# Kernel tuning notes

Hardware: AMD Instinct MI355X
Metric: run time of the kernel (lower is better)

The kernel has to match this reference:

```python
import jax, jax.numpy as jnp
import numpy as np

N, E = 50000, 600000
DIMS = [128, 256, 256, 256, 256, 64]  # in, h1..h4, out


def setup_inputs() -> dict:
    key = jax.random.key(0)
    ks = jax.random.split(key, 12)
    inp = {
        "x": jax.random.normal(ks[0], (N, DIMS[0]), dtype=jnp.float32),
        "edge_index": jax.random.randint(ks[1], (2, E), 0, N, dtype=jnp.int64 if jax.config.jax_enable_x64 else jnp.int32),
    }
    for i in range(5):
        fi, fo = DIMS[i], DIMS[i + 1]
        s = 1.0 / np.sqrt(fi)  # glorot-ish uniform, matching GCNConv default scale
        inp[f"W{i+1}"] = jax.random.uniform(ks[2 + 2 * i], (fi, fo), jnp.float32, -s, s)
        inp[f"b{i+1}"] = jnp.zeros((fo,), jnp.float32)
    return inp


def _gcn_norm(edge_index, n):
    # Add self-loops and compute symmetric normalization D^-1/2 (A+I) D^-1/2.
    loop = jnp.arange(n, dtype=edge_index.dtype)
    src = jnp.concatenate([edge_index[0], loop])  # [E+N]
    dst = jnp.concatenate([edge_index[1], loop])
    deg = jax.ops.segment_sum(jnp.ones_like(dst, dtype=jnp.float32), dst, num_segments=n)
    dinv = jnp.where(deg > 0, jax.lax.rsqrt(deg), 0.0)
    norm = dinv[src] * dinv[dst]  # [E+N]
    return src, dst, norm


def _gcn_layer(x, src, dst, norm, W, b, n):
    h = x @ W                       # [N, Fo] linear transform first (fewer msg bytes)
    msg = h[src] * norm[:, None]    # gather + edge-weight scale
    out = jax.ops.segment_sum(msg, dst, num_segments=n)  # scatter-add aggregate
    return out + b


def reference(x, edge_index, W1, b1, W2, b2, W3, b3, W4, b4, W5, b5):
    n = x.shape[0]
    src, dst, norm = _gcn_norm(edge_index, n)
    params = [(W1, b1), (W2, b2), (W3, b3), (W4, b4), (W5, b5)]
    h = x
    for i, (W, b) in enumerate(params):
        h = _gcn_layer(h, src, dst, norm, W, b, n)
        if i < 4:
            h = jax.nn.relu(h)  # dropout is identity in eval mode
    return h
```

## Files before the change

kernel.cpp:

```cpp
#include <hip/hip_runtime.h>
#include <stdint.h>


typedef _Float16 v8h __attribute__((ext_vector_type(8)));
typedef _Float16 v4h __attribute__((ext_vector_type(4)));
typedef _Float16 v2h __attribute__((ext_vector_type(2)));
typedef float v4f __attribute__((ext_vector_type(4)));

__global__ void count_edges(const int* __restrict__ dst, int E, int* __restrict__ counts) {
    int i = blockIdx.x * blockDim.x + threadIdx.x;
    if (i < E) atomicAdd(&counts[dst[i]], 1);
}

__global__ void block_sums(const int* __restrict__ counts, int n, int* __restrict__ partial) {
    __shared__ int red[256];
    int t = threadIdx.x;
    int i = blockIdx.x * 256 + t;
    red[t] = (i < n) ? counts[i] : 0;
    __syncthreads();
    #pragma unroll
    for (int off = 128; off > 0; off >>= 1) {
        if (t < off) red[t] += red[t + off];
        __syncthreads();
    }
    if (t == 0) partial[blockIdx.x] = red[0];
}

__global__ void scan_partials(int* __restrict__ partial, int nb, int* __restrict__ row_ptr, int n) {
    __shared__ int s[256];
    int t = threadIdx.x;
    int v = (t < nb) ? partial[t] : 0;
    s[t] = v;
    __syncthreads();
    #pragma unroll
    for (int off = 1; off < 256; off <<= 1) {
        int u = (t >= off) ? s[t - off] : 0;
        __syncthreads();
        s[t] += u;
        __syncthreads();
    }
    if (t < nb) partial[t] = s[t] - v;
    if (t == 0) row_ptr[n] = s[255];
}

__global__ void scan_final(const int* __restrict__ counts, int n, const int* __restrict__ partial,
                           int* __restrict__ row_ptr, float* __restrict__ dinv,
                           int* __restrict__ fill) {
    __shared__ int s[256];
    int t = threadIdx.x;
    int i = blockIdx.x * 256 + t;
    int c = (i < n) ? counts[i] : 0;
    s[t] = c;
    __syncthreads();
    #pragma unroll
    for (int off = 1; off < 256; off <<= 1) {
        int u = (t >= off) ? s[t - off] : 0;
        __syncthreads();
        s[t] += u;
        __syncthreads();
    }
    if (i < n) {
        row_ptr[i] = partial[blockIdx.x] + s[t] - c;
        dinv[i] = rsqrtf((float)(c + 1));
        fill[i] = 0;
    }
}

__global__ void build_csr(const int* __restrict__ src, const int* __restrict__ dst, int E,
                          const int* __restrict__ row_ptr, int* __restrict__ fill,
                          int2* __restrict__ esw, const float* __restrict__ dinv) {
    int i = blockIdx.x * blockDim.x + threadIdx.x;
    if (i < E) {
        int d = dst[i];
        int s = src[i];
        int pos = row_ptr[d] + atomicAdd(&fill[d], 1);
        esw[pos] = make_int2(s, __float_as_int(dinv[s]));
    }
}

struct SplitArgs {
    const float* W[5];
    _Float16* Wh[5];
    _Float16* Wl[5];
    int lgFI[5];
    int FO[5];
    int off[6];
};

__global__ void split_all(SplitArgs a) {
    int i = blockIdx.x * 256 + threadIdx.x;
    #pragma unroll
    for (int l = 0; l < 5; ++l) {
        if (i >= a.off[l] && i < a.off[l + 1]) {
            int j = i - a.off[l];
            int FI = 1 << a.lgFI[l];
            int c = j >> a.lgFI[l];
            int k = j & (FI - 1);
            float v = a.W[l][(size_t)k * a.FO[l] + c];
            _Float16 h = (_Float16)v;
            a.Wh[l][j] = h;
            a.Wl[l][j] = (_Float16)(v - (float)h);
        }
    }
}

__global__ __launch_bounds__(256) void agg_packed(
    const _Float16* __restrict__ inP, const int* __restrict__ row_ptr,
    const int2* __restrict__ esw, const float* __restrict__ dinv,
    _Float16* __restrict__ outH, _Float16* __restrict__ outL, int n) {
    int wid = (blockIdx.x * blockDim.x + threadIdx.x) >> 6;
    if (wid >= n) return;
    const int lane = threadIdx.x & 63;
    int e = __builtin_amdgcn_readfirstlane(row_ptr[wid]);
    const int end = __builtin_amdgcn_readfirstlane(row_ptr[wid + 1]);
    const float dd = dinv[wid];
    const _Float16* rb = inP + (size_t)lane * 8;
    float a0, a1, a2, a3;
    {
        v8h p = *(const v8h*)(rb + (size_t)wid * 512);
        a0 = dd * ((float)p[0] + (float)p[1]);
        a1 = dd * ((float)p[2] + (float)p[3]);
        a2 = dd * ((float)p[4] + (float)p[5]);
        a3 = dd * ((float)p[6] + (float)p[7]);
    }
#define GTH(q) (*(const v8h*)(rb + (size_t)(q).x * 512))
#define ACC(b, w)                                  \
    a0 += (w) * ((float)(b)[0] + (float)(b)[1]);   \
    a1 += (w) * ((float)(b)[2] + (float)(b)[3]);   \
    a2 += (w) * ((float)(b)[4] + (float)(b)[5]);   \
    a3 += (w) * ((float)(b)[6] + (float)(b)[7]);
    for (; e + 8 <= end; e += 8) {
        int2 q0 = esw[e + 0], q1 = esw[e + 1], q2 = esw[e + 2], q3 = esw[e + 3];
        int2 q4 = esw[e + 4], q5 = esw[e + 5], q6 = esw[e + 6], q7 = esw[e + 7];
        v8h b0 = GTH(q0), b1 = GTH(q1), b2 = GTH(q2), b3 = GTH(q3);
        v8h b4 = GTH(q4), b5 = GTH(q5), b6 = GTH(q6), b7 = GTH(q7);
        ACC(b0, __int_as_float(q0.y)) ACC(b1, __int_as_float(q1.y))
        ACC(b2, __int_as_float(q2.y)) ACC(b3, __int_as_float(q3.y))
        ACC(b4, __int_as_float(q4.y)) ACC(b5, __int_as_float(q5.y))
        ACC(b6, __int_as_float(q6.y)) ACC(b7, __int_as_float(q7.y))
    }
    if (e + 4 <= end) {
        int2 q0 = esw[e + 0], q1 = esw[e + 1], q2 = esw[e + 2], q3 = esw[e + 3];
        v8h b0 = GTH(q0), b1 = GTH(q1), b2 = GTH(q2), b3 = GTH(q3);
        ACC(b0, __int_as_float(q0.y)) ACC(b1, __int_as_float(q1.y))
        ACC(b2, __int_as_float(q2.y)) ACC(b3, __int_as_float(q3.y))
        e += 4;
    }
    if (e < end) {
        const int em = end - 1;
        int e1 = (e + 1 < end) ? e + 1 : em;
        int e2 = (e + 2 < end) ? e + 2 : em;
        int2 q0 = esw[e], q1 = esw[e1], q2 = esw[e2], q3 = esw[em];
        float w0 = __int_as_float(q0.y);
        float w1 = (e + 1 < end) ? __int_as_float(q1.y) : 0.f;
        float w2 = (e + 2 < end) ? __int_as_float(q2.y) : 0.f;
        float w3 = (e + 3 < end) ? __int_as_float(q3.y) : 0.f;
        v8h b0 = GTH(q0), b1 = GTH(q1), b2 = GTH(q2), b3 = GTH(q3);
        ACC(b0, w0) ACC(b1, w1) ACC(b2, w2) ACC(b3, w3)
    }
#undef GTH
#undef ACC
    size_t o = (size_t)wid * 256 + lane * 4;
    float s0 = dd * a0, s1 = dd * a1, s2 = dd * a2, s3 = dd * a3;
    _Float16 h0 = (_Float16)s0, h1 = (_Float16)s1, h2 = (_Float16)s2, h3 = (_Float16)s3;
    *(v4h*)&outH[o] = (v4h){h0, h1, h2, h3};
    *(v4h*)&outL[o] = (v4h){(_Float16)(s0 - (float)h0), (_Float16)(s1 - (float)h1),
                            (_Float16)(s2 - (float)h2), (_Float16)(s3 - (float)h3)};
}

__global__ __launch_bounds__(256) void agg_f32_128(
    const float* __restrict__ in, const int* __restrict__ row_ptr,
    const int2* __restrict__ esw, const float* __restrict__ dinv,
    _Float16* __restrict__ outH, _Float16* __restrict__ outL, int n) {
    int wid = (blockIdx.x * blockDim.x + threadIdx.x) >> 6;
    if (wid >= n) return;
    const int lane = threadIdx.x & 63;
    int e = __builtin_amdgcn_readfirstlane(row_ptr[wid]);
    const int end = __builtin_amdgcn_readfirstlane(row_ptr[wid + 1]);
    const float dd = dinv[wid];
    const float* rb = in + (size_t)lane * 2;
    float a0, a1;
    {
        float2 p = *(const float2*)(rb + (size_t)wid * 128);
        a0 = dd * p.x;
        a1 = dd * p.y;
    }
#define GTH(q) (*(const float2*)(rb + (size_t)(q).x * 128))
#define ACC(b, w) a0 += (w) * (b).x; a1 += (w) * (b).y;
    for (; e + 8 <= end; e += 8) {
        int2 q0 = esw[e + 0], q1 = esw[e + 1], q2 = esw[e + 2], q3 = esw[e + 3];
        int2 q4 = esw[e + 4], q5 = esw[e + 5], q6 = esw[e + 6], q7 = esw[e + 7];
        float2 b0 = GTH(q0), b1 = GTH(q1), b2 = GTH(q2), b3 = GTH(q3);
        float2 b4 = GTH(q4), b5 = GTH(q5), b6 = GTH(q6), b7 = GTH(q7);
        ACC(b0, __int_as_float(q0.y)) ACC(b1, __int_as_float(q1.y))
        ACC(b2, __int_as_float(q2.y)) ACC(b3, __int_as_float(q3.y))
        ACC(b4, __int_as_float(q4.y)) ACC(b5, __int_as_float(q5.y))
        ACC(b6, __int_as_float(q6.y)) ACC(b7, __int_as_float(q7.y))
    }
    if (e + 4 <= end) {
        int2 q0 = esw[e + 0], q1 = esw[e + 1], q2 = esw[e + 2], q3 = esw[e + 3];
        float2 b0 = GTH(q0), b1 = GTH(q1), b2 = GTH(q2), b3 = GTH(q3);
        ACC(b0, __int_as_float(q0.y)) ACC(b1, __int_as_float(q1.y))
        ACC(b2, __int_as_float(q2.y)) ACC(b3, __int_as_float(q3.y))
        e += 4;
    }
    if (e < end) {
        const int em = end - 1;
        int e1 = (e + 1 < end) ? e + 1 : em;
        int e2 = (e + 2 < end) ? e + 2 : em;
        int2 q0 = esw[e], q1 = esw[e1], q2 = esw[e2], q3 = esw[em];
        float w0 = __int_as_float(q0.y);
        float w1 = (e + 1 < end) ? __int_as_float(q1.y) : 0.f;
        float w2 = (e + 2 < end) ? __int_as_float(q2.y) : 0.f;
        float w3 = (e + 3 < end) ? __int_as_float(q3.y) : 0.f;
        float2 b0 = GTH(q0), b1 = GTH(q1), b2 = GTH(q2), b3 = GTH(q3);
        ACC(b0, w0) ACC(b1, w1) ACC(b2, w2) ACC(b3, w3)
    }
#undef GTH
#undef ACC
    size_t o = (size_t)wid * 128 + lane * 2;
    float s0 = dd * a0, s1 = dd * a1;
    _Float16 h0 = (_Float16)s0, h1 = (_Float16)s1;
    *(v2h*)&outH[o] = (v2h){h0, h1};
    *(v2h*)&outL[o] = (v2h){(_Float16)(s0 - (float)h0), (_Float16)(s1 - (float)h1)};
}

__global__ __launch_bounds__(256) void agg_f32_64(
    const float* __restrict__ in, const int* __restrict__ row_ptr,
    const int2* __restrict__ esw, const float* __restrict__ dinv,
    const float* __restrict__ bias, float* __restrict__ outF, int n) {
    int wid = (blockIdx.x * blockDim.x + threadIdx.x) >> 6;
    if (wid >= n) return;
    const int lane = threadIdx.x & 63;
    int e = __builtin_amdgcn_readfirstlane(row_ptr[wid]);
    const int end = __builtin_amdgcn_readfirstlane(row_ptr[wid + 1]);
    const float dd = dinv[wid];
    const float* rb = in + lane;
    float a0 = dd * rb[(size_t)wid * 64];
#define GTH(q) (rb[(size_t)(q).x * 64])
    for (; e + 8 <= end; e += 8) {
        int2 q0 = esw[e + 0], q1 = esw[e + 1], q2 = esw[e + 2], q3 = esw[e + 3];
        int2 q4 = esw[e + 4], q5 = esw[e + 5], q6 = esw[e + 6], q7 = esw[e + 7];
        float b0 = GTH(q0), b1 = GTH(q1), b2 = GTH(q2), b3 = GTH(q3);
        float b4 = GTH(q4), b5 = GTH(q5), b6 = GTH(q6), b7 = GTH(q7);
        a0 += __int_as_float(q0.y) * b0 + __int_as_float(q1.y) * b1;
        a0 += __int_as_float(q2.y) * b2 + __int_as_float(q3.y) * b3;
        a0 += __int_as_float(q4.y) * b4 + __int_as_float(q5.y) * b5;
        a0 += __int_as_float(q6.y) * b6 + __int_as_float(q7.y) * b7;
    }
    if (e + 4 <= end) {
        int2 q0 = esw[e + 0], q1 = esw[e + 1], q2 = esw[e + 2], q3 = esw[e + 3];
        float b0 = GTH(q0), b1 = GTH(q1), b2 = GTH(q2), b3 = GTH(q3);
        a0 += __int_as_float(q0.y) * b0 + __int_as_float(q1.y) * b1;
        a0 += __int_as_float(q2.y) * b2 + __int_as_float(q3.y) * b3;
        e += 4;
    }
    if (e < end) {
        const int em = end - 1;
        int e1 = (e + 1 < end) ? e + 1 : em;
        int e2 = (e + 2 < end) ? e + 2 : em;
        int2 q0 = esw[e], q1 = esw[e1], q2 = esw[e2], q3 = esw[em];
        float w0 = __int_as_float(q0.y);
        float w1 = (e + 1 < end) ? __int_as_float(q1.y) : 0.f;
        float w2 = (e + 2 < end) ? __int_as_float(q2.y) : 0.f;
        float w3 = (e + 3 < end) ? __int_as_float(q3.y) : 0.f;
        float b0 = GTH(q0), b1 = GTH(q1), b2 = GTH(q2), b3 = GTH(q3);
        a0 += w0 * b0 + w1 * b1 + w2 * b2 + w3 * b3;
    }
#undef GTH
    outF[(size_t)wid * 64 + lane] = dd * a0 + bias[lane];
}

__device__ __forceinline__ void gl_lds16(const _Float16* g, _Float16* l) {
    __builtin_amdgcn_global_load_lds(
        (const __attribute__((address_space(1))) uint32_t*)g,
        (__attribute__((address_space(3))) uint32_t*)l, 16, 0, 0);
}

template <int FI, int OUTMODE>
__global__ __launch_bounds__(256) void gemm_wide(
    const _Float16* __restrict__ Ah, const _Float16* __restrict__ Al,
    const _Float16* __restrict__ Wth, const _Float16* __restrict__ Wtl,
    const float* __restrict__ bias,
    uint32_t* __restrict__ Opk, _Float16* __restrict__ Oh, _Float16* __restrict__ Ol,
    int n) {
    constexpr int BK = 32;
    constexpr int NSTEP = FI / BK;
    __shared__ _Float16 lds[20480];
    const int m0 = blockIdx.x * 64;
    const int t = threadIdx.x;
    const int w = t >> 6;
    const int lane = t & 63;

    const int G = w * 64 + lane;
    const int arow = (G >> 6) * 16 + (G & 15), akc = ((G >> 4) & 3) * 8;
    const _Float16* sAh = Ah + (size_t)(m0 + arow) * FI + akc;
    const _Float16* sAl = Al + (size_t)(m0 + arow) * FI + akc;
    _Float16* dAh = &lds[w * 512];
    _Float16* dAl = &lds[2048 + w * 512];
    const int bq = lane & 15, bk = (lane >> 4) * 8;
    const _Float16* sB[4];
    _Float16* dBh[4];
    _Float16* dBl[4];
    #pragma unroll
    for (int q = 0; q < 4; ++q) {
        int sub = w * 4 + q;
        sB[q] = (const _Float16*)((size_t)(sub * 16 + bq) * FI + bk);
        dBh[q] = &lds[4096 + sub * 512];
        dBl[q] = &lds[12288 + sub * 512];
    }

    v4f acc[4][4];
    #pragma unroll
    for (int i = 0; i < 4; ++i)
        #pragma unroll
        for (int j = 0; j < 4; ++j) acc[i][j] = (v4f){0.f, 0.f, 0.f, 0.f};

    for (int s = 0; s < NSTEP; ++s) {
        const int ko = s * BK;
        gl_lds16(sAh + ko, dAh);
        gl_lds16(sAl + ko, dAl);
        #pragma unroll
        for (int q = 0; q < 4; ++q) {
            size_t off = (size_t)sB[q];
            gl_lds16(Wth + off + ko, dBh[q]);
            gl_lds16(Wtl + off + ko, dBl[q]);
        }
        __syncthreads();
        v8h ahf[4], alf[4], bhf[4], blf[4];
        #pragma unroll
        for (int i = 0; i < 4; ++i) {
            ahf[i] = *(const v8h*)&lds[i * 512 + lane * 8];
            alf[i] = *(const v8h*)&lds[2048 + i * 512 + lane * 8];
        }
        #pragma unroll
        for (int j = 0; j < 4; ++j) {
            bhf[j] = *(const v8h*)&lds[4096 + (w * 4 + j) * 512 + lane * 8];
            blf[j] = *(const v8h*)&lds[12288 + (w * 4 + j) * 512 + lane * 8];
        }
        #pragma unroll
        for (int i = 0; i < 4; ++i)
            #pragma unroll
            for (int j = 0; j < 4; ++j) {
                acc[i][j] = __builtin_amdgcn_mfma_f32_16x16x32_f16(ahf[i], bhf[j], acc[i][j], 0, 0, 0);
                acc[i][j] = __builtin_amdgcn_mfma_f32_16x16x32_f16(ahf[i], blf[j], acc[i][j], 0, 0, 0);
                acc[i][j] = __builtin_amdgcn_mfma_f32_16x16x32_f16(alf[i], bhf[j], acc[i][j], 0, 0, 0);
            }
        __syncthreads();
    }

    const int rl = (lane >> 4) * 4;
    const int cl = lane & 15;
    #pragma unroll
    for (int j = 0; j < 4; ++j) {
        const int gcol = w * 64 + j * 16 + cl;
        const float bv = bias[gcol];
        #pragma unroll
        for (int i = 0; i < 4; ++i) {
            const int grow = m0 + i * 16 + rl;
            #pragma unroll
            for (int r = 0; r < 4; ++r) {
                if (grow + r < n) {
                    float v = fmaxf(acc[i][j][r] + bv, 0.f);
                    _Float16 h = (_Float16)v;
                    _Float16 l = (_Float16)(v - (float)h);
                    if (OUTMODE == 0) {
                        uint32_t u = (uint32_t)__builtin_bit_cast(uint16_t, h) |
                                     ((uint32_t)__builtin_bit_cast(uint16_t, l) << 16);
                        Opk[(size_t)(grow + r) * 256 + gcol] = u;
                    } else {
                        Oh[(size_t)(grow + r) * 256 + gcol] = h;
                        Ol[(size_t)(grow + r) * 256 + gcol] = l;
                    }
                }
            }
        }
    }
}

__global__ __launch_bounds__(256) void gemm_narrow(
    const _Float16* __restrict__ Ah, const _Float16* __restrict__ Al,
    const _Float16* __restrict__ Wth, const _Float16* __restrict__ Wtl,
    float* __restrict__ Of, int n) {
    constexpr int FI = 256, FO = 64;
    __shared__ _Float16 lds[12288];
    const int m0 = blockIdx.x * 128;
    const int t = threadIdx.x;
    const int w = t >> 6;
    const int lane = t & 63;

    const int G0 = w * 128 + lane;
    const int G1 = G0 + 64;
    const int arow0 = (G0 >> 6) * 16 + (G0 & 15), akc0 = ((G0 >> 4) & 3) * 8;
    const int arow1 = (G1 >> 6) * 16 + (G1 & 15), akc1 = ((G1 >> 4) & 3) * 8;
    const _Float16* sAh0 = Ah + (size_t)(m0 + arow0) * FI + akc0;
    const _Float16* sAh1 = Ah + (size_t)(m0 + arow1) * FI + akc1;
    const _Float16* sAl0 = Al + (size_t)(m0 + arow0) * FI + akc0;
    const _Float16* sAl1 = Al + (size_t)(m0 + arow1) * FI + akc1;
    const int bcol = w * 16 + (lane & 15), bkc = (lane >> 4) * 8;
    const _Float16* sBh = Wth + (size_t)bcol * FI + bkc;
    const _Float16* sBl = Wtl + (size_t)bcol * FI + bkc;

    _Float16* dAh0 = &lds[w * 1024];
    _Float16* dAh1 = &lds[w * 1024 + 512];
    _Float16* dAl0 = &lds[4096 + w * 1024];
    _Float16* dAl1 = &lds[4096 + w * 1024 + 512];
    _Float16* dBh = &lds[8192 + w * 512];
    _Float16* dBl = &lds[10240 + w * 512];

    const int wm = w >> 1, wn = w & 1;
    v4f acc[4][2];
    #pragma unroll
    for (int i = 0; i < 4; ++i)
        #pragma unroll
        for (int j = 0; j < 2; ++j) acc[i][j] = (v4f){0.f, 0.f, 0.f, 0.f};

    for (int s = 0; s < 8; ++s) {
        const int ko = s * 32;
        gl_lds16(sAh0 + ko, dAh0);
        gl_lds16(sAh1 + ko, dAh1);
        gl_lds16(sAl0 + ko, dAl0);
        gl_lds16(sAl1 + ko, dAl1);
        gl_lds16(sBh + ko, dBh);
        gl_lds16(sBl + ko, dBl);
        __syncthreads();
        v8h ah[4], al[4], bh[2], bl[2];
        #pragma unroll
        for (int i = 0; i < 4; ++i) {
            ah[i] = *(const v8h*)&lds[(wm * 4 + i) * 512 + lane * 8];
            al[i] = *(const v8h*)&lds[4096 + (wm * 4 + i) * 512 + lane * 8];
        }
        #pragma unroll
        for (int j = 0; j < 2; ++j) {
            bh[j] = *(const v8h*)&lds[8192 + (wn * 2 + j) * 512 + lane * 8];
            bl[j] = *(const v8h*)&lds[10240 + (wn * 2 + j) * 512 + lane * 8];
        }
        #pragma unroll
        for (int i = 0; i < 4; ++i)
            #pragma unroll
            for (int j = 0; j < 2; ++j) {
                acc[i][j] = __builtin_amdgcn_mfma_f32_16x16x32_f16(ah[i], bh[j], acc[i][j], 0, 0, 0);
                acc[i][j] = __builtin_amdgcn_mfma_f32_16x16x32_f16(ah[i], bl[j], acc[i][j], 0, 0, 0);
                acc[i][j] = __builtin_amdgcn_mfma_f32_16x16x32_f16(al[i], bh[j], acc[i][j], 0, 0, 0);
            }
        __syncthreads();
    }

    const int rl = (lane >> 4) * 4;
    const int cl = lane & 15;
    #pragma unroll
    for (int j = 0; j < 2; ++j) {
        const int gcol = wn * 32 + j * 16 + cl;
        #pragma unroll
        for (int i = 0; i < 4; ++i) {
            const int grow = m0 + wm * 64 + i * 16 + rl;
            #pragma unroll
            for (int r = 0; r < 4; ++r)
                if (grow + r < n) Of[(size_t)(grow + r) * FO + gcol] = acc[i][j][r];
        }
    }
}

extern "C" void kernel_launch(void* const* d_in, const int* in_sizes, int n_in,
                              void* d_out, int out_size, void* d_ws, size_t ws_size,
                              hipStream_t stream) {
    const float* x = (const float*)d_in[0];
    const int* ei = (const int*)d_in[1];
    const int E = in_sizes[1] / 2;
    const int n = in_sizes[0] / 128;
    const int* esrc = ei;
    const int* edst = ei + E;
    const float* b[5] = {(const float*)d_in[3], (const float*)d_in[5], (const float*)d_in[7],
                         (const float*)d_in[9], (const float*)d_in[11]};
    float* out = (float*)d_out;
    const int NPAD = ((n + 127) / 128) * 128;

    char* ws = (char*)d_ws;
    auto carve = [&](size_t bytes) {
        char* p = ws;
        ws += (bytes + 255) & ~(size_t)255;
        return p;
    };
    int* counts = (int*)carve((size_t)n * 4);
    int* row_ptr = (int*)carve((size_t)(n + 1) * 4);
    int* fill = (int*)carve((size_t)n * 4);
    float* dinv = (float*)carve((size_t)n * 4);
    int* partial = (int*)carve(1024);
    int2* esw = (int2*)carve((size_t)E * 8);
    const int FIs[5] = {128, 256, 256, 256, 256};
    const int FOs[5] = {256, 256, 256, 256, 64};
    _Float16 *Wh[5], *Wl[5];
    for (int l = 0; l < 5; ++l) {
        Wh[l] = (_Float16*)carve((size_t)FIs[l] * FOs[l] * 2);
        Wl[l] = (_Float16*)carve((size_t)FIs[l] * FOs[l] * 2);
    }
    _Float16* Ah = (_Float16*)carve((size_t)NPAD * 256 * 2);
    _Float16* Al = (_Float16*)carve((size_t)NPAD * 256 * 2);
    uint32_t* Ppk = (uint32_t*)carve((size_t)NPAD * 256 * 4);
    _Float16* Bh2 = (_Float16*)Ppk;
    _Float16* Bl2 = (_Float16*)Ppk + (size_t)NPAD * 256;
    float* scratch = (float*)Ah;

    hipMemsetAsync(counts, 0, (size_t)n * 4, stream);
    count_edges<<<(E + 255) / 256, 256, 0, stream>>>(edst, E, counts);
    const int nsb = (n + 255) / 256;
    block_sums<<<nsb, 256, 0, stream>>>(counts, n, partial);
    scan_partials<<<1, 256, 0, stream>>>(partial, nsb, row_ptr, n);
    scan_final<<<nsb, 256, 0, stream>>>(counts, n, partial, row_ptr, dinv, fill);
    build_csr<<<(E + 255) / 256, 256, 0, stream>>>(esrc, edst, E, row_ptr, fill, esw, dinv);

    SplitArgs sa;
    int off = 0;
    for (int l = 0; l < 5; ++l) {
        sa.W[l] = (const float*)d_in[2 + 2 * l];
        sa.Wh[l] = Wh[l];
        sa.Wl[l] = Wl[l];
        sa.lgFI[l] = (FIs[l] == 128) ? 7 : 8;
        sa.FO[l] = FOs[l];
        sa.off[l] = off;
        off += FIs[l] * FOs[l];
    }
    sa.off[5] = off;
    split_all<<<(off + 255) / 256, 256, 0, stream>>>(sa);

    const int aggBlocks = (n + 3) / 4;
    const int gw = NPAD / 64;
    const int gn = NPAD / 128;

    agg_f32_128<<<aggBlocks, 256, 0, stream>>>(x, row_ptr, esw, dinv, Ah, Al, n);
    gemm_wide<128, 0><<<gw, 256, 0, stream>>>(Ah, Al, Wh[0], Wl[0], b[0], Ppk, nullptr, nullptr, n);
    for (int l = 1; l <= 2; ++l) {
        agg_packed<<<aggBlocks, 256, 0, stream>>>((const _Float16*)Ppk, row_ptr, esw, dinv, Ah, Al, n);
        gemm_wide<256, 0><<<gw, 256, 0, stream>>>(Ah, Al, Wh[l], Wl[l], b[l], Ppk, nullptr, nullptr, n);
    }
    agg_packed<<<aggBlocks, 256, 0, stream>>>((const _Float16*)Ppk, row_ptr, esw, dinv, Ah, Al, n);
    gemm_wide<256, 1><<<gw, 256, 0, stream>>>(Ah, Al, Wh[3], Wl[3], b[3], nullptr, Bh2, Bl2, n);
    gemm_narrow<<<gn, 256, 0, stream>>>(Bh2, Bl2, Wh[4], Wl[4], scratch, n);
    agg_f32_64<<<aggBlocks, 256, 0, stream>>>(scratch, row_ptr, esw, dinv, b[4], out, n);
}
```

Measured before the change: 669.5 us.

## Fuse sparse aggregation with dense GEMM per layer via LDS-staged tiles

Replaces the separate aggregation and wide GEMM kernels for layers 1-4 with one fused kernel. Each block aggregates 32 node rows straight into swizzled LDS as split fp16 hi/lo values, then runs the MFMA GEMM with bias and ReLU on those rows. This removes the global round trip of the aggregated Ah/Al buffers and halves the launch count. In exchange each block covers fewer rows, uses a large LDS allocation that can limit occupancy, and the gather phase runs serially before the GEMM with no overlap. Ping-pong buffers P0/P1 are used because a layer cannot overwrite its own input.

```diff
diff --git a/kernel.cpp b/kernel.cpp
--- a/kernel.cpp
+++ b/kernel.cpp
@@ -104,125 +104,301 @@
     }
 }
 
-__global__ __launch_bounds__(256) void agg_packed(
-    const _Float16* __restrict__ inP, const int* __restrict__ row_ptr,
+__device__ __forceinline__ void gl_lds16(const _Float16* g, _Float16* l) {
+    __builtin_amdgcn_global_load_lds(
+        (const __attribute__((address_space(1))) uint32_t*)g,
+        (__attribute__((address_space(3))) uint32_t*)l, 16, 0, 0);
+}
+
+template <int FI, int INMODE, int OUTMODE>
+__global__ __launch_bounds__(256) void layer_fused(
+    const void* __restrict__ in, const int* __restrict__ row_ptr,
     const int2* __restrict__ esw, const float* __restrict__ dinv,
-    _Float16* __restrict__ outH, _Float16* __restrict__ outL, int n) {
-    int wid = (blockIdx.x * blockDim.x + threadIdx.x) >> 6;
-    if (wid >= n) return;
-    const int lane = threadIdx.x & 63;
-    int e = __builtin_amdgcn_readfirstlane(row_ptr[wid]);
-    const int end = __builtin_amdgcn_readfirstlane(row_ptr[wid + 1]);
-    const float dd = dinv[wid];
-    const _Float16* rb = inP + (size_t)lane * 8;
-    float a0, a1, a2, a3;
-    {
-        v8h p = *(const v8h*)(rb + (size_t)wid * 512);
-        a0 = dd * ((float)p[0] + (float)p[1]);
-        a1 = dd * ((float)p[2] + (float)p[3]);
-        a2 = dd * ((float)p[4] + (float)p[5]);
-        a3 = dd * ((float)p[6] + (float)p[7]);
-    }
-#define GTH(q) (*(const v8h*)(rb + (size_t)(q).x * 512))
-#define ACC(b, w)                                  \
-    a0 += (w) * ((float)(b)[0] + (float)(b)[1]);   \
-    a1 += (w) * ((float)(b)[2] + (float)(b)[3]);   \
-    a2 += (w) * ((float)(b)[4] + (float)(b)[5]);   \
-    a3 += (w) * ((float)(b)[6] + (float)(b)[7]);
-    for (; e + 8 <= end; e += 8) {
-        int2 q0 = esw[e + 0], q1 = esw[e + 1], q2 = esw[e + 2], q3 = esw[e + 3];
-        int2 q4 = esw[e + 4], q5 = esw[e + 5], q6 = esw[e + 6], q7 = esw[e + 7];
-        v8h b0 = GTH(q0), b1 = GTH(q1), b2 = GTH(q2), b3 = GTH(q3);
-        v8h b4 = GTH(q4), b5 = GTH(q5), b6 = GTH(q6), b7 = GTH(q7);
-        ACC(b0, __int_as_float(q0.y)) ACC(b1, __int_as_float(q1.y))
-        ACC(b2, __int_as_float(q2.y)) ACC(b3, __int_as_float(q3.y))
-        ACC(b4, __int_as_float(q4.y)) ACC(b5, __int_as_float(q5.y))
-        ACC(b6, __int_as_float(q6.y)) ACC(b7, __int_as_float(q7.y))
-    }
-    if (e + 4 <= end) {
-        int2 q0 = esw[e + 0], q1 = esw[e + 1], q2 = esw[e + 2], q3 = esw[e + 3];
-        v8h b0 = GTH(q0), b1 = GTH(q1), b2 = GTH(q2), b3 = GTH(q3);
-        ACC(b0, __int_as_float(q0.y)) ACC(b1, __int_as_float(q1.y))
-        ACC(b2, __int_as_float(q2.y)) ACC(b3, __int_as_float(q3.y))
-        e += 4;
-    }
-    if (e < end) {
-        const int em = end - 1;
-        int e1 = (e + 1 < end) ? e + 1 : em;
-        int e2 = (e + 2 < end) ? e + 2 : em;
-        int2 q0 = esw[e], q1 = esw[e1], q2 = esw[e2], q3 = esw[em];
-        float w0 = __int_as_float(q0.y);
-        float w1 = (e + 1 < end) ? __int_as_float(q1.y) : 0.f;
-        float w2 = (e + 2 < end) ? __int_as_float(q2.y) : 0.f;
-        float w3 = (e + 3 < end) ? __int_as_float(q3.y) : 0.f;
-        v8h b0 = GTH(q0), b1 = GTH(q1), b2 = GTH(q2), b3 = GTH(q3);
-        ACC(b0, w0) ACC(b1, w1) ACC(b2, w2) ACC(b3, w3)
-    }
+    const _Float16* __restrict__ Wth, const _Float16* __restrict__ Wtl,
+    const float* __restrict__ bias,
+    uint32_t* __restrict__ Opk, _Float16* __restrict__ Oh, _Float16* __restrict__ Ol,
+    int n) {
+    constexpr int ALO = 32 * FI;
+    constexpr int BH = 64 * FI;
+    constexpr int BL = 64 * FI + 8192;
+    constexpr int NSTEP = FI / 32;
+    __shared__ _Float16 lds[64 * FI + 16384];
+    const int m0 = blockIdx.x * 32;
+    const int t = threadIdx.x;
+    const int w = t >> 6;
+    const int lane = t & 63;
+
+    for (int q = 0; q < 8; ++q) {
+        const int r = w * 8 + q;
+        const int grow = m0 + r;
+        if constexpr (INMODE == 1) {
+            float s0 = 0.f, s1 = 0.f, s2 = 0.f, s3 = 0.f;
+            if (grow < n) {
+                const _Float16* rb = (const _Float16*)in + (size_t)lane * 8;
+                int e = __builtin_amdgcn_readfirstlane(row_ptr[grow]);
+                const int end = __builtin_amdgcn_readfirstlane(row_ptr[grow + 1]);
+                const float dd = dinv[grow];
+                float a0, a1, a2, a3;
+                {
+                    v8h p = *(const v8h*)(rb + (size_t)grow * 512);
+                    a0 = dd * ((float)p[0] + (float)p[1]);
+                    a1 = dd * ((float)p[2] + (float)p[3]);
+                    a2 = dd * ((float)p[4] + (float)p[5]);
+                    a3 = dd * ((float)p[6] + (float)p[7]);
+                }
+#define GTH(qq) (*(const v8h*)(rb + (size_t)(qq).x * 512))
+#define ACC(b, wv)                                   \
+    a0 += (wv) * ((float)(b)[0] + (float)(b)[1]);    \
+    a1 += (wv) * ((float)(b)[2] + (float)(b)[3]);    \
+    a2 += (wv) * ((float)(b)[4] + (float)(b)[5]);    \
+    a3 += (wv) * ((float)(b)[6] + (float)(b)[7]);
+                for (; e + 8 <= end; e += 8) {
+                    int2 q0 = esw[e + 0], q1 = esw[e + 1], q2 = esw[e + 2], q3 = esw[e + 3];
+                    int2 q4 = esw[e + 4], q5 = esw[e + 5], q6 = esw[e + 6], q7 = esw[e + 7];
+                    v8h b0 = GTH(q0), b1 = GTH(q1), b2 = GTH(q2), b3 = GTH(q3);
+                    v8h b4 = GTH(q4), b5 = GTH(q5), b6 = GTH(q6), b7 = GTH(q7);
+                    ACC(b0, __int_as_float(q0.y)) ACC(b1, __int_as_float(q1.y))
+                    ACC(b2, __int_as_float(q2.y)) ACC(b3, __int_as_float(q3.y))
+                    ACC(b4, __int_as_float(q4.y)) ACC(b5, __int_as_float(q5.y))
+                    ACC(b6, __int_as_float(q6.y)) ACC(b7, __int_as_float(q7.y))
+                }
+                if (e + 4 <= end) {
+                    int2 q0 = esw[e + 0], q1 = esw[e + 1], q2 = esw[e + 2], q3 = esw[e + 3];
+                    v8h b0 = GTH(q0), b1 = GTH(q1), b2 = GTH(q2), b3 = GTH(q3);
+                    ACC(b0, __int_as_float(q0.y)) ACC(b1, __int_as_float(q1.y))
+                    ACC(b2, __int_as_float(q2.y)) ACC(b3, __int_as_float(q3.y))
+                    e += 4;
+                }
+                if (e < end) {
+                    const int em = end - 1;
+                    int e1 = (e + 1 < end) ? e + 1 : em;
+                    int e2 = (e + 2 < end) ? e + 2 : em;
+                    int2 q0 = esw[e], q1 = esw[e1], q2 = esw[e2], q3 = esw[em];
+                    float w0 = __int_as_float(q0.y);
+                    float w1 = (e + 1 < end) ? __int_as_float(q1.y) : 0.f;
+                    float w2 = (e + 2 < end) ? __int_as_float(q2.y) : 0.f;
+                    float w3 = (e + 3 < end) ? __int_as_float(q3.y) : 0.f;
+                    v8h b0 = GTH(q0), b1 = GTH(q1), b2 = GTH(q2), b3 = GTH(q3);
+                    ACC(b0, w0) ACC(b1, w1) ACC(b2, w2) ACC(b3, w3)
+                }
 #undef GTH
 #undef ACC
-    size_t o = (size_t)wid * 256 + lane * 4;
-    float s0 = dd * a0, s1 = dd * a1, s2 = dd * a2, s3 = dd * a3;
-    _Float16 h0 = (_Float16)s0, h1 = (_Float16)s1, h2 = (_Float16)s2, h3 = (_Float16)s3;
-    *(v4h*)&outH[o] = (v4h){h0, h1, h2, h3};
-    *(v4h*)&outL[o] = (v4h){(_Float16)(s0 - (float)h0), (_Float16)(s1 - (float)h1),
-                            (_Float16)(s2 - (float)h2), (_Float16)(s3 - (float)h3)};
-}
-
-__global__ __launch_bounds__(256) void agg_f32_128(
-    const float* __restrict__ in, const int* __restrict__ row_ptr,
-    const int2* __restrict__ esw, const float* __restrict__ dinv,
-    _Float16* __restrict__ outH, _Float16* __restrict__ outL, int n) {
-    int wid = (blockIdx.x * blockDim.x + threadIdx.x) >> 6;
-    if (wid >= n) return;
-    const int lane = threadIdx.x & 63;
-    int e = __builtin_amdgcn_readfirstlane(row_ptr[wid]);
-    const int end = __builtin_amdgcn_readfirstlane(row_ptr[wid + 1]);
-    const float dd = dinv[wid];
-    const float* rb = in + (size_t)lane * 2;
-    float a0, a1;
-    {
-        float2 p = *(const float2*)(rb + (size_t)wid * 128);
-        a0 = dd * p.x;
-        a1 = dd * p.y;
-    }
-#define GTH(q) (*(const float2*)(rb + (size_t)(q).x * 128))
-#define ACC(b, w) a0 += (w) * (b).x; a1 += (w) * (b).y;
-    for (; e + 8 <= end; e += 8) {
-        int2 q0 = esw[e + 0], q1 = esw[e + 1], q2 = esw[e + 2], q3 = esw[e + 3];
-        int2 q4 = esw[e + 4], q5 = esw[e + 5], q6 = esw[e + 6], q7 = esw[e + 7];
-        float2 b0 = GTH(q0), b1 = GTH(q1), b2 = GTH(q2), b3 = GTH(q3);
-        float2 b4 = GTH(q4), b5 = GTH(q5), b6 = GTH(q6), b7 = GTH(q7);
-        ACC(b0, __int_as_float(q0.y)) ACC(b1, __int_as_float(q1.y))
-        ACC(b2, __int_as_float(q2.y)) ACC(b3, __int_as_float(q3.y))
-        ACC(b4, __int_as_float(q4.y)) ACC(b5, __int_as_float(q5.y))
-        ACC(b6, __int_as_float(q6.y)) ACC(b7, __int_as_float(q7.y))
-    }
-    if (e + 4 <= end) {
-        int2 q0 = esw[e + 0], q1 = esw[e + 1], q2 = esw[e + 2], q3 = esw[e + 3];
-        float2 b0 = GTH(q0), b1 = GTH(q1), b2 = GTH(q2), b3 = GTH(q3);
-        ACC(b0, __int_as_float(q0.y)) ACC(b1, __int_as_float(q1.y))
-        ACC(b2, __int_as_float(q2.y)) ACC(b3, __int_as_float(q3.y))
-        e += 4;
-    }
-    if (e < end) {
-        const int em = end - 1;
-        int e1 = (e + 1 < end) ? e + 1 : em;
-        int e2 = (e + 2 < end) ? e + 2 : em;
-        int2 q0 = esw[e], q1 = esw[e1], q2 = esw[e2], q3 = esw[em];
-        float w0 = __int_as_float(q0.y);
-        float w1 = (e + 1 < end) ? __int_as_float(q1.y) : 0.f;
-        float w2 = (e + 2 < end) ? __int_as_float(q2.y) : 0.f;
-        float w3 = (e + 3 < end) ? __int_as_float(q3.y) : 0.f;
-        float2 b0 = GTH(q0), b1 = GTH(q1), b2 = GTH(q2), b3 = GTH(q3);
-        ACC(b0, w0) ACC(b1, w1) ACC(b2, w2) ACC(b3, w3)
-    }
+                s0 = dd * a0; s1 = dd * a1; s2 = dd * a2; s3 = dd * a3;
+            }
+            _Float16 h0 = (_Float16)s0, h1 = (_Float16)s1, h2 = (_Float16)s2, h3 = (_Float16)s3;
+            const int idx = (r * 256 + lane * 4) ^ ((r & 7) << 3);
+            *(v4h*)&lds[idx] = (v4h){h0, h1, h2, h3};
+            *(v4h*)&lds[ALO + idx] = (v4h){(_Float16)(s0 - (float)h0), (_Float16)(s1 - (float)h1),
+                                           (_Float16)(s2 - (float)h2), (_Float16)(s3 - (float)h3)};
+        } else {
+            float s0 = 0.f, s1 = 0.f;
+            if (grow < n) {
+                const float* rb = (const float*)in + (size_t)lane * 2;
+                int e = __builtin_amdgcn_readfirstlane(row_ptr[grow]);
+                const int end = __builtin_amdgcn_readfirstlane(row_ptr[grow + 1]);
+                const float dd = dinv[grow];
+                float a0, a1;
+                {
+                    float2 p = *(const float2*)(rb + (size_t)grow * 128);
+                    a0 = dd * p.x;
+                    a1 = dd * p.y;
+                }
+#define GTH(qq) (*(const float2*)(rb + (size_t)(qq).x * 128))
+#define ACC(b, wv) a0 += (wv) * (b).x; a1 += (wv) * (b).y;
+                for (; e + 8 <= end; e += 8) {
+                    int2 q0 = esw[e + 0], q1 = esw[e + 1], q2 = esw[e + 2], q3 = esw[e + 3];
+                    int2 q4 = esw[e + 4], q5 = esw[e + 5], q6 = esw[e + 6], q7 = esw[e + 7];
+                    float2 b0 = GTH(q0), b1 = GTH(q1), b2 = GTH(q2), b3 = GTH(q3);
+                    float2 b4 = GTH(q4), b5 = GTH(q5), b6 = GTH(q6), b7 = GTH(q7);
+                    ACC(b0, __int_as_float(q0.y)) ACC(b1, __int_as_float(q1.y))
+                    ACC(b2, __int_as_float(q2.y)) ACC(b3, __int_as_float(q3.y))
+                    ACC(b4, __int_as_float(q4.y)) ACC(b5, __int_as_float(q5.y))
+                    ACC(b6, __int_as_float(q6.y)) ACC(b7, __int_as_float(q7.y))
+                }
+                if (e + 4 <= end) {
+                    int2 q0 = esw[e + 0], q1 = esw[e + 1], q2 = esw[e + 2], q3 = esw[e + 3];
+                    float2 b0 = GTH(q0), b1 = GTH(q1), b2 = GTH(q2), b3 = GTH(q3);
+                    ACC(b0, __int_as_float(q0.y)) ACC(b1, __int_as_float(q1.y))
+                    ACC(b2, __int_as_float(q2.y)) ACC(b3, __int_as_float(q3.y))
+                    e += 4;
+                }
+                if (e < end) {
+                    const int em = end - 1;
+                    int e1 = (e + 1 < end) ? e + 1 : em;
+                    int e2 = (e + 2 < end) ? e + 2 : em;
+                    int2 q0 = esw[e], q1 = esw[e1], q2 = esw[e2], q3 = esw[em];
+                    float w0 = __int_as_float(q0.y);
+                    float w1 = (e + 1 < end) ? __int_as_float(q1.y) : 0.f;
+                    float w2 = (e + 2 < end) ? __int_as_float(q2.y) : 0.f;
+                    float w3 = (e + 3 < end) ? __int_as_float(q3.y) : 0.f;
+                    float2 b0 = GTH(q0), b1 = GTH(q1), b2 = GTH(q2), b3 = GTH(q3);
+                    ACC(b0, w0) ACC(b1, w1) ACC(b2, w2) ACC(b3, w3)
+                }
 #undef GTH
 #undef ACC
-    size_t o = (size_t)wid * 128 + lane * 2;
-    float s0 = dd * a0, s1 = dd * a1;
-    _Float16 h0 = (_Float16)s0, h1 = (_Float16)s1;
-    *(v2h*)&outH[o] = (v2h){h0, h1};
-    *(v2h*)&outL[o] = (v2h){(_Float16)(s0 - (float)h0), (_Float16)(s1 - (float)h1)};
+                s0 = dd * a0; s1 = dd * a1;
+            }
+            _Float16 h0 = (_Float16)s0, h1 = (_Float16)s1;
+            const int idx = (r * 128 + lane * 2) ^ ((r & 7) << 3);
+            *(v2h*)&lds[idx] = (v2h){h0, h1};
+            *(v2h*)&lds[ALO + idx] = (v2h){(_Float16)(s0 - (float)h0), (_Float16)(s1 - (float)h1)};
+        }
+    }
+    __syncthreads();
+
+    size_t boff[4];
+    #pragma unroll
+    for (int q = 0; q < 4; ++q)
+        boff[q] = (size_t)((w * 4 + q) * 16 + (lane & 15)) * FI + ((lane >> 4) * 8);
+
+    v4f acc[2][4];
+    #pragma unroll
+    for (int i = 0; i < 2; ++i)
+        #pragma unroll
+        for (int j = 0; j < 4; ++j) acc[i][j] = (v4f){0.f, 0.f, 0.f, 0.f};
+
+    for (int s = 0; s < NSTEP; ++s) {
+        const int ko = s * 32;
+        #pragma unroll
+        for (int q = 0; q < 4; ++q) {
+            gl_lds16(Wth + boff[q] + ko, &lds[BH + (w * 4 + q) * 512]);
+            gl_lds16(Wtl + boff[q] + ko, &lds[BL + (w * 4 + q) * 512]);
+        }
+        __syncthreads();
+        v8h ahf[2], alf[2], bhf[4], blf[4];
+        #pragma unroll
+        for (int i = 0; i < 2; ++i) {
+            const int ri = i * 16 + (lane & 15);
+            const int aidx = (ri * FI + ko + ((lane >> 4) << 3)) ^ ((lane & 7) << 3);
+            ahf[i] = *(const v8h*)&lds[aidx];
+            alf[i] = *(const v8h*)&lds[ALO + aidx];
+        }
+        #pragma unroll
+        for (int j = 0; j < 4; ++j) {
+            bhf[j] = *(const v8h*)&lds[BH + (w * 4 + j) * 512 + lane * 8];
+            blf[j] = *(const v8h*)&lds[BL + (w * 4 + j) * 512 + lane * 8];
+        }
+        #pragma unroll
+        for (int i = 0; i < 2; ++i)
+            #pragma unroll
+            for (int j = 0; j < 4; ++j) {
+                acc[i][j] = __builtin_amdgcn_mfma_f32_16x16x32_f16(ahf[i], bhf[j], acc[i][j], 0, 0, 0);
+                acc[i][j] = __builtin_amdgcn_mfma_f32_16x16x32_f16(ahf[i], blf[j], acc[i][j], 0, 0, 0);
+                acc[i][j] = __builtin_amdgcn_mfma_f32_16x16x32_f16(alf[i], bhf[j], acc[i][j], 0, 0, 0);
+            }
+        __syncthreads();
+    }
+
+    const int rl = (lane >> 4) * 4;
+    const int cl = lane & 15;
+    #pragma unroll
+    for (int j = 0; j < 4; ++j) {
+        const int gcol = w * 64 + j * 16 + cl;
+        const float bv = bias[gcol];
+        #pragma unroll
+        for (int i = 0; i < 2; ++i) {
+            const int growb = m0 + i * 16 + rl;
+            #pragma unroll
+            for (int r = 0; r < 4; ++r) {
+                if (growb + r < n) {
+                    float v = fmaxf(acc[i][j][r] + bv, 0.f);
+                    _Float16 h = (_Float16)v;
+                    _Float16 l = (_Float16)(v - (float)h);
+                    if (OUTMODE == 0) {
+                        uint32_t u = (uint32_t)__builtin_bit_cast(uint16_t, h) |
+                                     ((uint32_t)__builtin_bit_cast(uint16_t, l) << 16);
+                        Opk[(size_t)(growb + r) * 256 + gcol] = u;
+                    } else {
+                        Oh[(size_t)(growb + r) * 256 + gcol] = h;
+                        Ol[(size_t)(growb + r) * 256 + gcol] = l;
+                    }
+                }
+            }
+        }
+    }
+}
+
+__global__ __launch_bounds__(256) void gemm_narrow(
+    const _Float16* __restrict__ Ah, const _Float16* __restrict__ Al,
+    const _Float16* __restrict__ Wth, const _Float16* __restrict__ Wtl,
+    float* __restrict__ Of, int n) {
+    constexpr int FI = 256, FO = 64;
+    __shared__ _Float16 lds[12288];
+    const int m0 = blockIdx.x * 128;
+    const int t = threadIdx.x;
+    const int w = t >> 6;
+    const int lane = t & 63;
+
+    const int G0 = w * 128 + lane;
+    const int G1 = G0 + 64;
+    const int arow0 = (G0 >> 6) * 16 + (G0 & 15), akc0 = ((G0 >> 4) & 3) * 8;
+    const int arow1 = (G1 >> 6) * 16 + (G1 & 15), akc1 = ((G1 >> 4) & 3) * 8;
+    const _Float16* sAh0 = Ah + (size_t)(m0 + arow0) * FI + akc0;
+    const _Float16* sAh1 = Ah + (size_t)(m0 + arow1) * FI + akc1;
+    const _Float16* sAl0 = Al + (size_t)(m0 + arow0) * FI + akc0;
+    const _Float16* sAl1 = Al + (size_t)(m0 + arow1) * FI + akc1;
+    const int bcol = w * 16 + (lane & 15), bkc = (lane >> 4) * 8;
+    const _Float16* sBh = Wth + (size_t)bcol * FI + bkc;
+    const _Float16* sBl = Wtl + (size_t)bcol * FI + bkc;
+
+    _Float16* dAh0 = &lds[w * 1024];
+    _Float16* dAh1 = &lds[w * 1024 + 512];
+    _Float16* dAl0 = &lds[4096 + w * 1024];
+    _Float16* dAl1 = &lds[4096 + w * 1024 + 512];
+    _Float16* dBh = &lds[8192 + w * 512];
+    _Float16* dBl = &lds[10240 + w * 512];
+
+    const int wm = w >> 1, wn = w & 1;
+    v4f acc[4][2];
+    #pragma unroll
+    for (int i = 0; i < 4; ++i)
+        #pragma unroll
+        for (int j = 0; j < 2; ++j) acc[i][j] = (v4f){0.f, 0.f, 0.f, 0.f};
+
+    for (int s = 0; s < 8; ++s) {
+        const int ko = s * 32;
+        gl_lds16(sAh0 + ko, dAh0);
+        gl_lds16(sAh1 + ko, dAh1);
+        gl_lds16(sAl0 + ko, dAl0);
+        gl_lds16(sAl1 + ko, dAl1);
+        gl_lds16(sBh + ko, dBh);
+        gl_lds16(sBl + ko, dBl);
+        __syncthreads();
+        v8h ah[4], al[4], bh[2], bl[2];
+        #pragma unroll
+        for (int i = 0; i < 4; ++i) {
+            ah[i] = *(const v8h*)&lds[(wm * 4 + i) * 512 + lane * 8];
+            al[i] = *(const v8h*)&lds[4096 + (wm * 4 + i) * 512 + lane * 8];
+        }
+        #pragma unroll
+        for (int j = 0; j < 2; ++j) {
+            bh[j] = *(const v8h*)&lds[8192 + (wn * 2 + j) * 512 + lane * 8];
+            bl[j] = *(const v8h*)&lds[10240 + (wn * 2 + j) * 512 + lane * 8];
+        }
+        #pragma unroll
+        for (int i = 0; i < 4; ++i)
+            #pragma unroll
+            for (int j = 0; j < 2; ++j) {
+                acc[i][j] = __builtin_amdgcn_mfma_f32_16x16x32_f16(ah[i], bh[j], acc[i][j], 0, 0, 0);
+                acc[i][j] = __builtin_amdgcn_mfma_f32_16x16x32_f16(ah[i], bl[j], acc[i][j], 0, 0, 0);
+                acc[i][j] = __builtin_amdgcn_mfma_f32_16x16x32_f16(al[i], bh[j], acc[i][j], 0, 0, 0);
+            }
+        __syncthreads();
+    }
+
+    const int rl = (lane >> 4) * 4;
+    const int cl = lane & 15;
+    #pragma unroll
+    for (int j = 0; j < 2; ++j) {
+        const int gcol = wn * 32 + j * 16 + cl;
+        #pragma unroll
+        for (int i = 0; i < 4; ++i) {
+            const int grow = m0 + wm * 64 + i * 16 + rl;
+            #pragma unroll
+            for (int r = 0; r < 4; ++r)
+                if (grow + r < n) Of[(size_t)(grow + r) * FO + gcol] = acc[i][j][r];
+        }
+    }
 }
 
 __global__ __launch_bounds__(256) void agg_f32_64(
@@ -271,196 +447,6 @@
     outF[(size_t)wid * 64 + lane] = dd * a0 + bias[lane];
 }
 
-__device__ __forceinline__ void gl_lds16(const _Float16* g, _Float16* l) {
-    __builtin_amdgcn_global_load_lds(
-        (const __attribute__((address_space(1))) uint32_t*)g,
-        (__attribute__((address_space(3))) uint32_t*)l, 16, 0, 0);
-}
-
-template <int FI, int OUTMODE>
-__global__ __launch_bounds__(256) void gemm_wide(
-    const _Float16* __restrict__ Ah, const _Float16* __restrict__ Al,
-    const _Float16* __restrict__ Wth, const _Float16* __restrict__ Wtl,
-    const float* __restrict__ bias,
-    uint32_t* __restrict__ Opk, _Float16* __restrict__ Oh, _Float16* __restrict__ Ol,
-    int n) {
-    constexpr int BK = 32;
-    constexpr int NSTEP = FI / BK;
-    __shared__ _Float16 lds[20480];
-    const int m0 = blockIdx.x * 64;
-    const int t = threadIdx.x;
-    const int w = t >> 6;
-    const int lane = t & 63;
-
-    const int G = w * 64 + lane;
-    const int arow = (G >> 6) * 16 + (G & 15), akc = ((G >> 4) & 3) * 8;
-    const _Float16* sAh = Ah + (size_t)(m0 + arow) * FI + akc;
-    const _Float16* sAl = Al + (size_t)(m0 + arow) * FI + akc;
-    _Float16* dAh = &lds[w * 512];
-    _Float16* dAl = &lds[2048 + w * 512];
-    const int bq = lane & 15, bk = (lane >> 4) * 8;
-    const _Float16* sB[4];
-    _Float16* dBh[4];
-    _Float16* dBl[4];
-    #pragma unroll
-    for (int q = 0; q < 4; ++q) {
-        int sub = w * 4 + q;
-        sB[q] = (const _Float16*)((size_t)(sub * 16 + bq) * FI + bk);
-        dBh[q] = &lds[4096 + sub * 512];
-        dBl[q] = &lds[12288 + sub * 512];
-    }
-
-    v4f acc[4][4];
-    #pragma unroll
-    for (int i = 0; i < 4; ++i)
-        #pragma unroll
-        for (int j = 0; j < 4; ++j) acc[i][j] = (v4f){0.f, 0.f, 0.f, 0.f};
-
-    for (int s = 0; s < NSTEP; ++s) {
-        const int ko = s * BK;
-        gl_lds16(sAh + ko, dAh);
-        gl_lds16(sAl + ko, dAl);
-        #pragma unroll
-        for (int q = 0; q < 4; ++q) {
-            size_t off = (size_t)sB[q];
-            gl_lds16(Wth + off + ko, dBh[q]);
-            gl_lds16(Wtl + off + ko, dBl[q]);
-        }
-        __syncthreads();
-        v8h ahf[4], alf[4], bhf[4], blf[4];
-        #pragma unroll
-        for (int i = 0; i < 4; ++i) {
-            ahf[i] = *(const v8h*)&lds[i * 512 + lane * 8];
-            alf[i] = *(const v8h*)&lds[2048 + i * 512 + lane * 8];
-        }
-        #pragma unroll
-        for (int j = 0; j < 4; ++j) {
-            bhf[j] = *(const v8h*)&lds[4096 + (w * 4 + j) * 512 + lane * 8];
-            blf[j] = *(const v8h*)&lds[12288 + (w * 4 + j) * 512 + lane * 8];
-        }
-        #pragma unroll
-        for (int i = 0; i < 4; ++i)
-            #pragma unroll
-            for (int j = 0; j < 4; ++j) {
-                acc[i][j] = __builtin_amdgcn_mfma_f32_16x16x32_f16(ahf[i], bhf[j], acc[i][j], 0, 0, 0);
-                acc[i][j] = __builtin_amdgcn_mfma_f32_16x16x32_f16(ahf[i], blf[j], acc[i][j], 0, 0, 0);
-                acc[i][j] = __builtin_amdgcn_mfma_f32_16x16x32_f16(alf[i], bhf[j], acc[i][j], 0, 0, 0);
-            }
-        __syncthreads();
-    }
-
-    const int rl = (lane >> 4) * 4;
-    const int cl = lane & 15;
-    #pragma unroll
-    for (int j = 0; j < 4; ++j) {
-        const int gcol = w * 64 + j * 16 + cl;
-        const float bv = bias[gcol];
-        #pragma unroll
-        for (int i = 0; i < 4; ++i) {
-            const int grow = m0 + i * 16 + rl;
-            #pragma unroll
-            for (int r = 0; r < 4; ++r) {
-                if (grow + r < n) {
-                    float v = fmaxf(acc[i][j][r] + bv, 0.f);
-                    _Float16 h = (_Float16)v;
-                    _Float16 l = (_Float16)(v - (float)h);
-                    if (OUTMODE == 0) {
-                        uint32_t u = (uint32_t)__builtin_bit_cast(uint16_t, h) |
-                                     ((uint32_t)__builtin_bit_cast(uint16_t, l) << 16);
-                        Opk[(size_t)(grow + r) * 256 + gcol] = u;
-                    } else {
-                        Oh[(size_t)(grow + r) * 256 + gcol] = h;
-                        Ol[(size_t)(grow + r) * 256 + gcol] = l;
-                    }
-                }
-            }
-        }
-    }
-}
-
-__global__ __launch_bounds__(256) void gemm_narrow(
-    const _Float16* __restrict__ Ah, const _Float16* __restrict__ Al,
-    const _Float16* __restrict__ Wth, const _Float16* __restrict__ Wtl,
-    float* __restrict__ Of, int n) {
-    constexpr int FI = 256, FO = 64;
-    __shared__ _Float16 lds[12288];
-    const int m0 = blockIdx.x * 128;
-    const int t = threadIdx.x;
-    const int w = t >> 6;
-    const int lane = t & 63;
-
-    const int G0 = w * 128 + lane;
-    const int G1 = G0 + 64;
-    const int arow0 = (G0 >> 6) * 16 + (G0 & 15), akc0 = ((G0 >> 4) & 3) * 8;
-    const int arow1 = (G1 >> 6) * 16 + (G1 & 15), akc1 = ((G1 >> 4) & 3) * 8;
-    const _Float16* sAh0 = Ah + (size_t)(m0 + arow0) * FI + akc0;
-    const _Float16* sAh1 = Ah + (size_t)(m0 + arow1) * FI + akc1;
-    const _Float16* sAl0 = Al + (size_t)(m0 + arow0) * FI + akc0;
-    const _Float16* sAl1 = Al + (size_t)(m0 + arow1) * FI + akc1;
-    const int bcol = w * 16 + (lane & 15), bkc = (lane >> 4) * 8;
-    const _Float16* sBh = Wth + (size_t)bcol * FI + bkc;
-    const _Float16* sBl = Wtl + (size_t)bcol * FI + bkc;
-
-    _Float16* dAh0 = &lds[w * 1024];
-    _Float16* dAh1 = &lds[w * 1024 + 512];
-    _Float16* dAl0 = &lds[4096 + w * 1024];
-    _Float16* dAl1 = &lds[4096 + w * 1024 + 512];
-    _Float16* dBh = &lds[8192 + w * 512];
-    _Float16* dBl = &lds[10240 + w * 512];
-
-    const int wm = w >> 1, wn = w & 1;
-    v4f acc[4][2];
-    #pragma unroll
-    for (int i = 0; i < 4; ++i)
-        #pragma unroll
-        for (int j = 0; j < 2; ++j) acc[i][j] = (v4f){0.f, 0.f, 0.f, 0.f};
-
-    for (int s = 0; s < 8; ++s) {
-        const int ko = s * 32;
-        gl_lds16(sAh0 + ko, dAh0);
-        gl_lds16(sAh1 + ko, dAh1);
-        gl_lds16(sAl0 + ko, dAl0);
-        gl_lds16(sAl1 + ko, dAl1);
-        gl_lds16(sBh + ko, dBh);
-        gl_lds16(sBl + ko, dBl);
-        __syncthreads();
-        v8h ah[4], al[4], bh[2], bl[2];
-        #pragma unroll
-        for (int i = 0; i < 4; ++i) {
-            ah[i] = *(const v8h*)&lds[(wm * 4 + i) * 512 + lane * 8];
-            al[i] = *(const v8h*)&lds[4096 + (wm * 4 + i) * 512 + lane * 8];
-        }
-        #pragma unroll
-        for (int j = 0; j < 2; ++j) {
-            bh[j] = *(const v8h*)&lds[8192 + (wn * 2 + j) * 512 + lane * 8];
-            bl[j] = *(const v8h*)&lds[10240 + (wn * 2 + j) * 512 + lane * 8];
-        }
-        #pragma unroll
-        for (int i = 0; i < 4; ++i)
-            #pragma unroll
-            for (int j = 0; j < 2; ++j) {
-                acc[i][j] = __builtin_amdgcn_mfma_f32_16x16x32_f16(ah[i], bh[j], acc[i][j], 0, 0, 0);
-                acc[i][j] = __builtin_amdgcn_mfma_f32_16x16x32_f16(ah[i], bl[j], acc[i][j], 0, 0, 0);
-                acc[i][j] = __builtin_amdgcn_mfma_f32_16x16x32_f16(al[i], bh[j], acc[i][j], 0, 0, 0);
-            }
-        __syncthreads();
-    }
-
-    const int rl = (lane >> 4) * 4;
-    const int cl = lane & 15;
-    #pragma unroll
-    for (int j = 0; j < 2; ++j) {
-        const int gcol = wn * 32 + j * 16 + cl;
-        #pragma unroll
-        for (int i = 0; i < 4; ++i) {
-            const int grow = m0 + wm * 64 + i * 16 + rl;
-            #pragma unroll
-            for (int r = 0; r < 4; ++r)
-                if (grow + r < n) Of[(size_t)(grow + r) * FO + gcol] = acc[i][j][r];
-        }
-    }
-}
-
 extern "C" void kernel_launch(void* const* d_in, const int* in_sizes, int n_in,
                               void* d_out, int out_size, void* d_ws, size_t ws_size,
                               hipStream_t stream) {
@@ -494,12 +480,11 @@
         Wh[l] = (_Float16*)carve((size_t)FIs[l] * FOs[l] * 2);
         Wl[l] = (_Float16*)carve((size_t)FIs[l] * FOs[l] * 2);
     }
-    _Float16* Ah = (_Float16*)carve((size_t)NPAD * 256 * 2);
-    _Float16* Al = (_Float16*)carve((size_t)NPAD * 256 * 2);
-    uint32_t* Ppk = (uint32_t*)carve((size_t)NPAD * 256 * 4);
-    _Float16* Bh2 = (_Float16*)Ppk;
-    _Float16* Bl2 = (_Float16*)Ppk + (size_t)NPAD * 256;
-    float* scratch = (float*)Ah;
+    uint32_t* P0 = (uint32_t*)carve((size_t)NPAD * 256 * 4);
+    uint32_t* P1 = (uint32_t*)carve((size_t)NPAD * 256 * 4);
+    _Float16* Bh2 = (_Float16*)P1;
+    _Float16* Bl2 = (_Float16*)P1 + (size_t)NPAD * 256;
+    float* scratch = (float*)P0;
 
     hipMemsetAsync(counts, 0, (size_t)n * 4, stream);
     count_edges<<<(E + 255) / 256, 256, 0, stream>>>(edst, E, counts);
@@ -523,18 +508,16 @@
     sa.off[5] = off;
     split_all<<<(off + 255) / 256, 256, 0, stream>>>(sa);
 
-    const int aggBlocks = (n + 3) / 4;
-    const int gw = NPAD / 64;
-    const int gn = NPAD / 128;
-
-    agg_f32_128<<<aggBlocks, 256, 0, stream>>>(x, row_ptr, esw, dinv, Ah, Al, n);
-    gemm_wide<128, 0><<<gw, 256, 0, stream>>>(Ah, Al, Wh[0], Wl[0], b[0], Ppk, nullptr, nullptr, n);
-    for (int l = 1; l <= 2; ++l) {
-        agg_packed<<<aggBlocks, 256, 0, stream>>>((const _Float16*)Ppk, row_ptr, esw, dinv, Ah, Al, n);
-        gemm_wide<256, 0><<<gw, 256, 0, stream>>>(Ah, Al, Wh[l], Wl[l], b[l], Ppk, nullptr, nullptr, n);
-    }
-    agg_packed<<<aggBlocks, 256, 0, stream>>>((const _Float16*)Ppk, row_ptr, esw, dinv, Ah, Al, n);
-    gemm_wide<256, 1><<<gw, 256, 0, stream>>>(Ah, Al, Wh[3], Wl[3], b[3], nullptr, Bh2, Bl2, n);
-    gemm_narrow<<<gn, 256, 0, stream>>>(Bh2, Bl2, Wh[4], Wl[4], scratch, n);
-    agg_f32_64<<<aggBlocks, 256, 0, stream>>>(scratch, row_ptr, esw, dinv, b[4], out, n);
-}
+    const int gf = NPAD / 32;
+
+    layer_fused<128, 0, 0><<<gf, 256, 0, stream>>>(x, row_ptr, esw, dinv, Wh[0], Wl[0], b[0],
+                                                   P0, nullptr, nullptr, n);
+    layer_fused<256, 1, 0><<<gf, 256, 0, stream>>>(P0, row_ptr, esw, dinv, Wh[1], Wl[1], b[1],
+                                                   P1, nullptr, nullptr, n);
+    layer_fused<256, 1, 0><<<gf, 256, 0, stream>>>(P1, row_ptr, esw, dinv, Wh[2], Wl[2], b[2],
+                                                   P0, nullptr, nullptr, n);
+    layer_fused<256, 1, 1><<<gf, 256, 0, stream>>>(P0, row_ptr, esw, dinv, Wh[3], Wl[3], b[3],
+                                                   nullptr, Bh2, Bl2, n);
+    gemm_narrow<<<NPAD / 128, 256, 0, stream>>>(Bh2, Bl2, Wh[4], Wl[4], scratch, n);
+    agg_f32_64<<<(n + 3) / 4, 256, 0, stream>>>(scratch, row_ptr, esw, dinv, b[4], out, n);
+}
```

Result: slower. 731.6 us (+9.3%).
